# Optimization experiments

Measured on AMD Instinct MI355X. Metric: run time of the kernel, lower is better.

Reference implementation:

```python
import jax, jax.numpy as jnp
import numpy as np

B, S, E, H = 8, 2048, 1024, 64

def setup_inputs() -> dict:
    key = jax.random.key(0)
    ks = jax.random.split(key, 10)
    inp = {
        'input_Q': jax.random.normal(ks[0], (B, S, E), dtype=jnp.float32),
        'input_K': jax.random.normal(ks[1], (B, S, E), dtype=jnp.float32),
        'input_V': jax.random.normal(ks[2], (B, S, E), dtype=jnp.float32),
        'mask': jax.random.randint(ks[3], (B, S, S), 0, 2) > 0,
        # Linear params: torch Linear(E, H) -> weight [H, E], use as x @ W^T + b; store transposed [E, H]
        'Wq': jax.random.normal(ks[4], (E, H), dtype=jnp.float32) / np.sqrt(E),
        'bq': jnp.zeros((H,), dtype=jnp.float32),
        'Wk': jax.random.normal(ks[5], (E, H), dtype=jnp.float32) / np.sqrt(E),
        'bk': jnp.zeros((H,), dtype=jnp.float32),
        'Wv': jax.random.normal(ks[6], (E, H), dtype=jnp.float32) / np.sqrt(E),
        'bv': jnp.zeros((H,), dtype=jnp.float32),
    }
    return inp

def reference(input_Q, input_K, input_V, mask, Wq, bq, Wk, bk, Wv, bv):
    Q = jnp.einsum('bse,eh->bsh', input_Q, Wq) + bq  # [B,S,H]
    K = jnp.einsum('bse,eh->bsh', input_K, Wk) + bk
    V = jnp.einsum('bse,eh->bsh', input_V, Wv) + bv
    scores = jnp.einsum('bqh,bkh->bqk', Q, K) / np.sqrt(H).astype(np.float32)  # [B,S,S]
    # faithful to masked_fill_(mask, 1e-10) BEFORE softmax
    scores = jnp.where(mask, jnp.float32(1e-10), scores)
    attn = jax.nn.softmax(scores, axis=-1)
    # dropout is identity in eval/reference mode
    return jnp.einsum('bqk,bkh->bqh', attn, V)
```

## Files before the change

kernel.cpp:

```cpp
#include <hip/hip_runtime.h>
#include <hip/hip_bf16.h>
#include <stdint.h>

constexpr int Bc = 8, Sc = 2048, Ec = 1024, Hc = 64;

typedef __bf16 bf16x8 __attribute__((ext_vector_type(8)));
typedef float f32x4 __attribute__((ext_vector_type(4)));
typedef unsigned short ushort8 __attribute__((ext_vector_type(8)));
typedef unsigned short ushort4v __attribute__((ext_vector_type(4)));

static __device__ __forceinline__ unsigned short f2bf(float f) {
  uint32_t u = __builtin_bit_cast(uint32_t, f);
  u = u + 0x7fffu + ((u >> 16) & 1u);
  return (unsigned short)(u >> 16);
}
static __device__ __forceinline__ bf16x8 ldb8(const unsigned short* p) {
  return __builtin_bit_cast(bf16x8, *(const ushort8*)p);
}

__global__ __launch_bounds__(256) void wt_kernel(
    const float* __restrict__ Wq, const float* __restrict__ Wk,
    const float* __restrict__ Wv, unsigned short* __restrict__ Wt) {
  int idx = blockIdx.x * 256 + threadIdx.x;
  int m = idx >> 16;
  int r = idx & 65535;
  int h = r >> 10;
  int e = r & 1023;
  const float* W = (m == 0) ? Wq : (m == 1) ? Wk : Wv;
  float scale = (m == 0) ? 0.125f : 1.0f;
  Wt[idx] = f2bf(W[e * Hc + h] * scale);
}

__global__ __launch_bounds__(256, 8) void proj_kernel(
    const float* __restrict__ Xq, const float* __restrict__ Xk,
    const float* __restrict__ Xv, const float* __restrict__ bq,
    const float* __restrict__ bk, const float* __restrict__ bv,
    const unsigned short* __restrict__ Wt,
    unsigned short* __restrict__ Qb, unsigned short* __restrict__ Kb,
    unsigned short* __restrict__ Vt) {
  const int mat = blockIdx.y;
  const float* X = (mat == 0) ? Xq : (mat == 1) ? Xk : Xv;
  const float* bias = (mat == 0) ? bq : (mat == 1) ? bk : bv;
  const float bscale = (mat == 0) ? 0.125f : 1.0f;
  const unsigned short* W = Wt + mat * (Hc * Ec);

  const int tid = threadIdx.x;
  const int wave = tid >> 6, lane = tid & 63;
  const int row0 = blockIdx.x * 16;
  const int arow = row0 + (lane & 15);
  const int kofs = (lane >> 4) * 8;

  const float* aptr = X + (size_t)arow * Ec + kofs;
  const unsigned short* wbase =
      W + (size_t)(wave * 16 + (lane & 15)) * Ec + kofs;

  f32x4 acc = (f32x4){0.f, 0.f, 0.f, 0.f};

  for (int kb = 0; kb < Ec; kb += 32) {
    float4 a0 = *(const float4*)(aptr + kb);
    float4 a1 = *(const float4*)(aptr + kb + 4);
    bf16x8 bfrag = ldb8(wbase + kb);
    ushort8 au;
    au[0] = f2bf(a0.x); au[1] = f2bf(a0.y); au[2] = f2bf(a0.z); au[3] = f2bf(a0.w);
    au[4] = f2bf(a1.x); au[5] = f2bf(a1.y); au[6] = f2bf(a1.z); au[7] = f2bf(a1.w);
    bf16x8 afrag = __builtin_bit_cast(bf16x8, au);
    acc = __builtin_amdgcn_mfma_f32_16x16x32_bf16(afrag, bfrag, acc, 0, 0, 0);
  }

  __shared__ unsigned short tile[16][72];
  {
    float bcol = bias[wave * 16 + (lane & 15)] * bscale;
#pragma unroll
    for (int r = 0; r < 4; r++)
      tile[(lane >> 4) * 4 + r][wave * 16 + (lane & 15)] = f2bf(acc[r] + bcol);
  }
  __syncthreads();

  if (mat < 2) {
    unsigned short* out = (mat == 0) ? Qb : Kb;
    int s_l = tid >> 4;
    int c0 = (tid & 15) * 4;
    ushort4v v = *(const ushort4v*)&tile[s_l][c0];
    *(ushort4v*)(out + (size_t)(row0 + s_l) * Hc + c0) = v;
  } else {
    int h = tid >> 2;
    int sc = (tid & 3) * 4;
    int bb = row0 >> 11;
    int sbase = (row0 & 2047) + sc;
    ushort4v v;
#pragma unroll
    for (int i = 0; i < 4; i++) v[i] = tile[sc + i][h];
    *(ushort4v*)(Vt + ((size_t)bb * Hc + h) * Sc + sbase) = v;
  }
}

__global__ __launch_bounds__(256, 4) void attn_kernel(
    const unsigned short* __restrict__ Qb, const unsigned short* __restrict__ Kb,
    const unsigned short* __restrict__ Vt, const int* __restrict__ mask,
    float* __restrict__ out) {
  const int b = blockIdx.y;
  const int q0 = blockIdx.x * 16;
  const int tid = threadIdx.x;
  const int wave = tid >> 6, lane = tid & 63;

  __shared__ unsigned short Ps[4][16][72];
  __shared__ float sm[4][16], sl[4][16];
  __shared__ float Os[4][16][64];

  const unsigned short* qptr =
      Qb + ((size_t)b * Sc + q0 + (lane & 15)) * Hc + (lane >> 4) * 8;
  bf16x8 aQ0 = ldb8(qptr);
  bf16x8 aQ1 = ldb8(qptr + 32);

  float m_r[4], l_r[4];
  f32x4 Oacc[4];
#pragma unroll
  for (int r = 0; r < 4; r++) { m_r[r] = -INFINITY; l_r[r] = 0.f; }
#pragma unroll
  for (int ht = 0; ht < 4; ht++) Oacc[ht] = (f32x4){0.f, 0.f, 0.f, 0.f};

  const int* mrow[4];
#pragma unroll
  for (int r = 0; r < 4; r++)
    mrow[r] = mask + ((size_t)b * Sc + q0 + (lane >> 4) * 4 + r) * Sc + (lane & 15);

  const unsigned short* kbase =
      Kb + ((size_t)b * Sc) * Hc + (size_t)(lane & 15) * Hc + (lane >> 4) * 8;
  const unsigned short* vbase[4];
#pragma unroll
  for (int ht = 0; ht < 4; ht++)
    vbase[ht] = Vt + ((size_t)b * Hc + ht * 16 + (lane & 15)) * Sc + (lane >> 4) * 8;

  for (int c = 0; c < 8; c++) {
    const int koff = wave * 512 + c * 64;

    int mv[4][4];
#pragma unroll
    for (int nt = 0; nt < 4; nt++)
#pragma unroll
      for (int r = 0; r < 4; r++) mv[nt][r] = mrow[r][koff + nt * 16];

    float sv[4][4];
#pragma unroll
    for (int nt = 0; nt < 4; nt++) {
      const unsigned short* kp = kbase + (size_t)(koff + nt * 16) * Hc;
      bf16x8 bK0 = ldb8(kp);
      bf16x8 bK1 = ldb8(kp + 32);
      f32x4 s = (f32x4){0.f, 0.f, 0.f, 0.f};
      s = __builtin_amdgcn_mfma_f32_16x16x32_bf16(aQ0, bK0, s, 0, 0, 0);
      s = __builtin_amdgcn_mfma_f32_16x16x32_bf16(aQ1, bK1, s, 0, 0, 0);
#pragma unroll
      for (int r = 0; r < 4; r++) sv[nt][r] = mv[nt][r] ? 1e-10f : s[r];
    }

    float rmax[4];
#pragma unroll
    for (int r = 0; r < 4; r++) {
      rmax[r] = fmaxf(fmaxf(sv[0][r], sv[1][r]), fmaxf(sv[2][r], sv[3][r]));
#pragma unroll
      for (int off = 1; off < 16; off <<= 1)
        rmax[r] = fmaxf(rmax[r], __shfl_xor(rmax[r], off, 64));
    }

    float alpha[4], p[4][4], psum[4];
#pragma unroll
    for (int r = 0; r < 4; r++) {
      float mnew = fmaxf(m_r[r], rmax[r]);
      alpha[r] = __expf(m_r[r] - mnew);
      m_r[r] = mnew;
      psum[r] = 0.f;
    }
#pragma unroll
    for (int nt = 0; nt < 4; nt++)
#pragma unroll
      for (int r = 0; r < 4; r++) {
        p[nt][r] = __expf(sv[nt][r] - m_r[r]);
        psum[r] += p[nt][r];
      }
#pragma unroll
    for (int r = 0; r < 4; r++) {
#pragma unroll
      for (int off = 1; off < 16; off <<= 1)
        psum[r] += __shfl_xor(psum[r], off, 64);
      l_r[r] = l_r[r] * alpha[r] + psum[r];
    }
#pragma unroll
    for (int ht = 0; ht < 4; ht++)
#pragma unroll
      for (int r = 0; r < 4; r++) Oacc[ht][r] *= alpha[r];

#pragma unroll
    for (int nt = 0; nt < 4; nt++)
#pragma unroll
      for (int r = 0; r < 4; r++)
        Ps[wave][(lane >> 4) * 4 + r][nt * 16 + (lane & 15)] = f2bf(p[nt][r]);

#pragma unroll
    for (int ks = 0; ks < 2; ks++) {
      bf16x8 aP = ldb8(&Ps[wave][lane & 15][ks * 32 + (lane >> 4) * 8]);
#pragma unroll
      for (int ht = 0; ht < 4; ht++) {
        bf16x8 bV = ldb8(vbase[ht] + koff + ks * 32);
        Oacc[ht] = __builtin_amdgcn_mfma_f32_16x16x32_bf16(aP, bV, Oacc[ht], 0, 0, 0);
      }
    }
  }

  if ((lane & 15) == 0) {
#pragma unroll
    for (int r = 0; r < 4; r++) {
      sm[wave][(lane >> 4) * 4 + r] = m_r[r];
      sl[wave][(lane >> 4) * 4 + r] = l_r[r];
    }
  }
  __syncthreads();

  float coef[4];
#pragma unroll
  for (int r = 0; r < 4; r++) {
    int row = (lane >> 4) * 4 + r;
    float M = fmaxf(fmaxf(sm[0][row], sm[1][row]), fmaxf(sm[2][row], sm[3][row]));
    coef[r] = __expf(m_r[r] - M);
  }
#pragma unroll
  for (int ht = 0; ht < 4; ht++)
#pragma unroll
    for (int r = 0; r < 4; r++)
      Os[wave][(lane >> 4) * 4 + r][ht * 16 + (lane & 15)] = Oacc[ht][r] * coef[r];
  __syncthreads();

  {
#pragma unroll
    for (int i = 0; i < 4; i++) {
      int row = wave * 4 + i;
      float M = fmaxf(fmaxf(sm[0][row], sm[1][row]), fmaxf(sm[2][row], sm[3][row]));
      float L = sl[0][row] * __expf(sm[0][row] - M) +
                sl[1][row] * __expf(sm[1][row] - M) +
                sl[2][row] * __expf(sm[2][row] - M) +
                sl[3][row] * __expf(sm[3][row] - M);
      float acc = Os[0][row][lane] + Os[1][row][lane] +
                  Os[2][row][lane] + Os[3][row][lane];
      out[((size_t)b * Sc + q0 + row) * Hc + lane] = acc / L;
    }
  }
}

extern "C" void kernel_launch(void* const* d_in, const int* in_sizes, int n_in,
                              void* d_out, int out_size, void* d_ws, size_t ws_size,
                              hipStream_t stream) {
  const float* Xq = (const float*)d_in[0];
  const float* Xk = (const float*)d_in[1];
  const float* Xv = (const float*)d_in[2];
  const int* mask = (const int*)d_in[3];
  const float* Wq = (const float*)d_in[4];
  const float* bq = (const float*)d_in[5];
  const float* Wk = (const float*)d_in[6];
  const float* bk = (const float*)d_in[7];
  const float* Wv = (const float*)d_in[8];
  const float* bv = (const float*)d_in[9];

  unsigned short* Qb = (unsigned short*)d_ws;
  unsigned short* Kb = Qb + (size_t)Bc * Sc * Hc;
  unsigned short* Vt = Kb + (size_t)Bc * Sc * Hc;
  unsigned short* Wt = Vt + (size_t)Bc * Sc * Hc;

  wt_kernel<<<dim3(3 * Hc * Ec / 256), 256, 0, stream>>>(Wq, Wk, Wv, Wt);
  proj_kernel<<<dim3(Bc * Sc / 16, 3), 256, 0, stream>>>(Xq, Xk, Xv, bq, bk, bv,
                                                         Wt, Qb, Kb, Vt);
  attn_kernel<<<dim3(Sc / 16, Bc), 256, 0, stream>>>(Qb, Kb, Vt, mask,
                                                     (float*)d_out);
}
```

Before: 441.0 us.

## Retile projection GEMM to 64-row blocks with LDS staging and register prefetch

The projection kernel now handles 64 rows per block instead of 16. X and W chunks are staged through shared memory, and each wave computes a 16x64 output tile with four accumulators. The next K-chunk is prefetched into registers while the current one is computed, so global loads overlap with MFMA work and each W element is read once per 64 rows instead of once per 16. This adds shared-memory use, a barrier per chunk and more registers, and the occupancy hint drops to 4 blocks.

```diff
diff --git a/kernel.cpp b/kernel.cpp
--- a/kernel.cpp
+++ b/kernel.cpp
@@ -16,6 +16,9 @@
 }
 static __device__ __forceinline__ bf16x8 ldb8(const unsigned short* p) {
   return __builtin_bit_cast(bf16x8, *(const ushort8*)p);
+}
+static __device__ __forceinline__ uint32_t pk2bf(float a, float b) {
+  return (uint32_t)f2bf(a) | ((uint32_t)f2bf(b) << 16);
 }
 
 __global__ __launch_bounds__(256) void wt_kernel(
@@ -31,7 +34,7 @@
   Wt[idx] = f2bf(W[e * Hc + h] * scale);
 }
 
-__global__ __launch_bounds__(256, 8) void proj_kernel(
+__global__ __launch_bounds__(256, 4) void proj_kernel(
     const float* __restrict__ Xq, const float* __restrict__ Xk,
     const float* __restrict__ Xv, const float* __restrict__ bq,
     const float* __restrict__ bk, const float* __restrict__ bv,
@@ -46,51 +49,98 @@
 
   const int tid = threadIdx.x;
   const int wave = tid >> 6, lane = tid & 63;
-  const int row0 = blockIdx.x * 16;
-  const int arow = row0 + (lane & 15);
-  const int kofs = (lane >> 4) * 8;
-
-  const float* aptr = X + (size_t)arow * Ec + kofs;
-  const unsigned short* wbase =
-      W + (size_t)(wave * 16 + (lane & 15)) * Ec + kofs;
-
-  f32x4 acc = (f32x4){0.f, 0.f, 0.f, 0.f};
-
-  for (int kb = 0; kb < Ec; kb += 32) {
-    float4 a0 = *(const float4*)(aptr + kb);
-    float4 a1 = *(const float4*)(aptr + kb + 4);
-    bf16x8 bfrag = ldb8(wbase + kb);
-    ushort8 au;
-    au[0] = f2bf(a0.x); au[1] = f2bf(a0.y); au[2] = f2bf(a0.z); au[3] = f2bf(a0.w);
-    au[4] = f2bf(a1.x); au[5] = f2bf(a1.y); au[6] = f2bf(a1.z); au[7] = f2bf(a1.w);
-    bf16x8 afrag = __builtin_bit_cast(bf16x8, au);
-    acc = __builtin_amdgcn_mfma_f32_16x16x32_bf16(afrag, bfrag, acc, 0, 0, 0);
-  }
-
-  __shared__ unsigned short tile[16][72];
-  {
-    float bcol = bias[wave * 16 + (lane & 15)] * bscale;
+  const int row0 = blockIdx.x * 64;
+
+  __shared__ unsigned short As[64][72];
+  __shared__ unsigned short Ws[64][72];
+
+  const int xrow = tid >> 4;
+  const int xcol = (tid & 15) * 4;
+  const float* xptr = X + (size_t)(row0 + xrow) * Ec + xcol;
+
+  float4 xr[4];
+  ushort8 wr[2];
+
+  auto load_chunk = [&](int c) {
+    const int k0 = c * 64;
+#pragma unroll
+    for (int p = 0; p < 4; p++)
+      xr[p] = *(const float4*)(xptr + (size_t)(p * 16) * Ec + k0);
+#pragma unroll
+    for (int i = 0; i < 2; i++) {
+      int j = i * 256 + tid;
+      int h = j >> 3, kg = j & 7;
+      wr[i] = *(const ushort8*)(W + (size_t)h * Ec + k0 + kg * 8);
+    }
+  };
+
+  f32x4 acc[4];
+#pragma unroll
+  for (int nt = 0; nt < 4; nt++) acc[nt] = (f32x4){0.f, 0.f, 0.f, 0.f};
+
+  load_chunk(0);
+
+  for (int c = 0; c < 16; c++) {
+#pragma unroll
+    for (int p = 0; p < 4; p++) {
+      ushort4v v = __builtin_bit_cast(
+          ushort4v, (uint2){pk2bf(xr[p].x, xr[p].y), pk2bf(xr[p].z, xr[p].w)});
+      *(ushort4v*)&As[p * 16 + xrow][xcol] = v;
+    }
+#pragma unroll
+    for (int i = 0; i < 2; i++) {
+      int j = i * 256 + tid;
+      *(ushort8*)&Ws[j >> 3][(j & 7) * 8] = wr[i];
+    }
+    __syncthreads();
+
+    if (c < 15) load_chunk(c + 1);
+
+#pragma unroll
+    for (int kk = 0; kk < 2; kk++) {
+      bf16x8 aA = ldb8(&As[wave * 16 + (lane & 15)][kk * 32 + (lane >> 4) * 8]);
+#pragma unroll
+      for (int nt = 0; nt < 4; nt++) {
+        bf16x8 bW = ldb8(&Ws[nt * 16 + (lane & 15)][kk * 32 + (lane >> 4) * 8]);
+        acc[nt] = __builtin_amdgcn_mfma_f32_16x16x32_bf16(aA, bW, acc[nt], 0, 0, 0);
+      }
+    }
+    __syncthreads();
+  }
+
+#pragma unroll
+  for (int nt = 0; nt < 4; nt++) {
+    float bcol = bias[nt * 16 + (lane & 15)] * bscale;
 #pragma unroll
     for (int r = 0; r < 4; r++)
-      tile[(lane >> 4) * 4 + r][wave * 16 + (lane & 15)] = f2bf(acc[r] + bcol);
+      As[wave * 16 + (lane >> 4) * 4 + r][nt * 16 + (lane & 15)] =
+          f2bf(acc[nt][r] + bcol);
   }
   __syncthreads();
 
   if (mat < 2) {
     unsigned short* out = (mat == 0) ? Qb : Kb;
-    int s_l = tid >> 4;
-    int c0 = (tid & 15) * 4;
-    ushort4v v = *(const ushort4v*)&tile[s_l][c0];
-    *(ushort4v*)(out + (size_t)(row0 + s_l) * Hc + c0) = v;
+    int s_l = tid >> 2;
+    int hs = (tid & 3) * 16;
+    ushort8 v0 = *(const ushort8*)&As[s_l][hs];
+    ushort8 v1 = *(const ushort8*)&As[s_l][hs + 8];
+    unsigned short* dst = out + (size_t)(row0 + s_l) * Hc + hs;
+    *(ushort8*)dst = v0;
+    *(ushort8*)(dst + 8) = v1;
   } else {
     int h = tid >> 2;
-    int sc = (tid & 3) * 4;
+    int ss = (tid & 3) * 16;
     int bb = row0 >> 11;
-    int sbase = (row0 & 2047) + sc;
-    ushort4v v;
-#pragma unroll
-    for (int i = 0; i < 4; i++) v[i] = tile[sc + i][h];
-    *(ushort4v*)(Vt + ((size_t)bb * Hc + h) * Sc + sbase) = v;
+    int sbase = (row0 & 2047) + ss;
+    ushort8 v0, v1;
+#pragma unroll
+    for (int i = 0; i < 8; i++) {
+      v0[i] = As[ss + i][h];
+      v1[i] = As[ss + 8 + i][h];
+    }
+    unsigned short* dst = Vt + ((size_t)bb * Hc + h) * Sc + sbase;
+    *(ushort8*)dst = v0;
+    *(ushort8*)(dst + 8) = v1;
   }
 }
 
@@ -265,7 +315,7 @@
   unsigned short* Wt = Vt + (size_t)Bc * Sc * Hc;
 
   wt_kernel<<<dim3(3 * Hc * Ec / 256), 256, 0, stream>>>(Wq, Wk, Wv, Wt);
-  proj_kernel<<<dim3(Bc * Sc / 16, 3), 256, 0, stream>>>(Xq, Xk, Xv, bq, bk, bv,
+  proj_kernel<<<dim3(Bc * Sc / 64, 3), 256, 0, stream>>>(Xq, Xk, Xv, bq, bk, bv,
                                                          Wt, Qb, Kb, Vt);
   attn_kernel<<<dim3(Sc / 16, Bc), 256, 0, stream>>>(Qb, Kb, Vt, mask,
                                                      (float*)d_out);
```

Result: faster. 380.4 us (-13.7%).
